# Performance work log

Hardware: AMD Instinct MI355X
Metric: run time of the kernel (lower is better)

The kernel has to match this reference:

```python
import jax, jax.numpy as jnp
import numpy as np

EMB = 256
HEADS = 2
IMG = 224
P1, P2 = 16, 8
LN_EPS = 1e-5


def _layer_norm(t, g, b):
    m = jnp.mean(t, axis=-1, keepdims=True)
    v = jnp.mean((t - m) ** 2, axis=-1, keepdims=True)
    return (t - m) * jax.lax.rsqrt(v + LN_EPS) * g + b


def _patch_embed(x, W, b, cls_tok, p):
    B, C, H, Wd = x.shape
    h, w = H // p, Wd // p
    # b c (h p1)(w p2) -> b (h w) (p1 p2 c)
    t = x.reshape(B, C, h, p, w, p).transpose(0, 2, 4, 3, 5, 1).reshape(B, h * w, p * p * C)
    t = t @ W + b
    cls = jnp.broadcast_to(cls_tok, (B, 1, cls_tok.shape[-1]))
    return jnp.concatenate([cls, t], axis=1)


def setup_inputs() -> dict:
    key = jax.random.key(0)
    ks = jax.random.split(key, 16)
    s = 0.02
    d = {
        "x": jax.random.normal(ks[0], (128, 3, IMG, IMG), dtype=jnp.float32),
        "W1": jax.random.normal(ks[1], (P1 * P1 * 3, EMB), dtype=jnp.float32) * s,
        "b1": jnp.zeros((EMB,), jnp.float32),
        "cls1": jax.random.normal(ks[2], (1, 1, EMB), dtype=jnp.float32),
        "W2": jax.random.normal(ks[3], (P2 * P2 * 3, EMB), dtype=jnp.float32) * s,
        "b2": jnp.zeros((EMB,), jnp.float32),
        "cls2": jax.random.normal(ks[4], (1, 1, EMB), dtype=jnp.float32),
        "ln1_g": jnp.ones((EMB,), jnp.float32),
        "ln1_b": jnp.zeros((EMB,), jnp.float32),
        "Wq": jax.random.normal(ks[5], (EMB, EMB), dtype=jnp.float32) * s,
        "bq": jnp.zeros((EMB,), jnp.float32),
        "Wk": jax.random.normal(ks[6], (EMB, EMB), dtype=jnp.float32) * s,
        "bk": jnp.zeros((EMB,), jnp.float32),
        "Wv": jax.random.normal(ks[7], (EMB, EMB), dtype=jnp.float32) * s,
        "bv": jnp.zeros((EMB,), jnp.float32),
        "Wp": jax.random.normal(ks[8], (EMB, EMB), dtype=jnp.float32) * s,
        "bp": jnp.zeros((EMB,), jnp.float32),
        "ln2_g": jnp.ones((EMB,), jnp.float32),
        "ln2_b": jnp.zeros((EMB,), jnp.float32),
        "lnc_g": jnp.ones((EMB,), jnp.float32),
        "lnc_b": jnp.zeros((EMB,), jnp.float32),
        "Wc": jax.random.normal(ks[9], (EMB, 2), dtype=jnp.float32) * s,
        "bc": jnp.zeros((2,), jnp.float32),
    }
    return d


def reference(x, W1, b1, cls1, W2, b2, cls2, ln1_g, ln1_b, Wq, bq, Wk, bk, Wv, bv,
              Wp, bp, ln2_g, ln2_b, lnc_g, lnc_b, Wc, bc):
    B = x.shape[0]
    p1 = _patch_embed(x, W1, b1, cls1, P1)   # [B, 197, 256]
    p2 = _patch_embed(x, W2, b2, cls2, P2)   # [B, 785, 256]
    n = p1.shape[1]
    idx = jnp.linspace(0.0, p2.shape[1] - 1, n).astype(jnp.int32)  # truncation like .long()
    p2r = p2[:, idx, :]
    z = jnp.concatenate([p2r, p1], axis=1)   # [B, 394, 256]
    N = z.shape[1]

    h = _layer_norm(z, ln1_g, ln1_b)
    dh = EMB // HEADS
    q = (h @ Wq + bq).reshape(B, N, HEADS, dh).transpose(0, 2, 1, 3)
    k = (h @ Wk + bk).reshape(B, N, HEADS, dh).transpose(0, 2, 1, 3)
    v = (h @ Wv + bv).reshape(B, N, HEADS, dh).transpose(0, 2, 1, 3)
    attn = jnp.einsum('bhqd,bhkd->bhqk', q, k)
    # NOTE: faithful to source — softmax of UNscaled logits, then divide by sqrt(emb)
    attn = jax.nn.softmax(attn, axis=-1) / (EMB ** 0.5)
    o = jnp.einsum('bhqk,bhkd->bhqd', attn, v).transpose(0, 2, 1, 3).reshape(B, N, EMB)
    o = o @ Wp + bp
    o = _layer_norm(o, ln2_g, ln2_b)
    z = z + o

    pooled = jnp.mean(z, axis=1)
    logits = _layer_norm(pooled, lnc_g, lnc_b) @ Wc + bc
    return jax.nn.log_softmax(logits, axis=1)
```

## Files before the change

### kernel.cpp

```cpp
#include <hip/hip_runtime.h>

typedef short short8 __attribute__((ext_vector_type(8)));
typedef float f32x4 __attribute__((ext_vector_type(4)));
typedef unsigned short us4 __attribute__((ext_vector_type(4)));
typedef unsigned short u16;

#define MFMA(a,b,c) __builtin_amdgcn_mfma_f32_16x16x32_bf16((a),(b),(c),0,0,0)

__device__ __forceinline__ u16 f2b(float f) {
    union { float f; unsigned int i; } v; v.f = f;
    unsigned int x = v.i;
    return (u16)((x + 0x7fffu + ((x >> 16) & 1u)) >> 16);
}

__device__ __forceinline__ unsigned int pk2(float lo, float hi) {
    return (unsigned int)f2b(lo) | ((unsigned int)f2b(hi) << 16);
}

__global__ __launch_bounds__(256) void k_wtrans(const float* __restrict__ W1,
        const float* __restrict__ W2, const float* __restrict__ Wq, const float* __restrict__ Wk,
        const float* __restrict__ Wv, const float* __restrict__ Wp,
        u16* __restrict__ w1t, u16* __restrict__ w2t, u16* __restrict__ wqt,
        u16* __restrict__ wkt, u16* __restrict__ wvt, u16* __restrict__ wpt) {
    int bx = blockIdx.x, n = threadIdx.x;
    if (bx < 768) {
        int k = bx, c = k % 3, t = k / 3, pj = t & 15, pi = t >> 4;
        int kp2 = c*256 + pi*16 + pj;
        w1t[(size_t)(kp2 >> 5)*8192 + n*32 + (kp2 & 31)] = f2b(W1[(size_t)k*256 + n]);
    } else if (bx < 960) {
        int k = bx - 768, c = k % 3, t = k / 3, pj = t & 7, pi = t >> 3;
        int kp2 = c*64 + pi*8 + pj;
        w2t[(size_t)(kp2 >> 5)*8192 + n*32 + (kp2 & 31)] = f2b(W2[(size_t)k*256 + n]);
    } else if (bx < 1216) { int k = bx - 960;  wqt[(size_t)(k>>5)*8192 + n*32 + (k&31)] = f2b(Wq[(size_t)k*256 + n]); }
    else if (bx < 1472)   { int k = bx - 1216; wkt[(size_t)(k>>5)*8192 + n*32 + (k&31)] = f2b(Wk[(size_t)k*256 + n]); }
    else if (bx < 1728)   { int k = bx - 1472; wvt[(size_t)(k>>5)*8192 + n*32 + (k&31)] = f2b(Wv[(size_t)k*256 + n]); }
    else                  { int k = bx - 1728; wpt[(size_t)(k>>5)*8192 + n*32 + (k&31)] = f2b(Wp[(size_t)k*256 + n]); }
}

__global__ __launch_bounds__(256) void k_cls(const float* __restrict__ cls1,
        const float* __restrict__ cls2, const float* __restrict__ g1, const float* __restrict__ be1,
        float* __restrict__ z, u16* __restrict__ h) {
    __shared__ float red[16];
    int b = blockIdx.x, e = threadIdx.x, lane = e & 63, w = e >> 6;
    float v0 = cls2[e], v1 = cls1[e];
    z[((size_t)b*394 + 0)*256 + e]   = v0;
    z[((size_t)b*394 + 197)*256 + e] = v1;
    float s0 = v0, q0 = v0*v0, s1 = v1, q1 = v1*v1;
    #pragma unroll
    for (int m = 1; m < 64; m <<= 1) {
        s0 += __shfl_xor(s0, m); q0 += __shfl_xor(q0, m);
        s1 += __shfl_xor(s1, m); q1 += __shfl_xor(q1, m);
    }
    if (lane == 0) { red[w] = s0; red[4+w] = q0; red[8+w] = s1; red[12+w] = q1; }
    __syncthreads();
    float S0 = red[0]+red[1]+red[2]+red[3],   Q0 = red[4]+red[5]+red[6]+red[7];
    float S1 = red[8]+red[9]+red[10]+red[11], Q1 = red[12]+red[13]+red[14]+red[15];
    float m0 = S0*(1.f/256.f), r0 = rsqrtf(Q0*(1.f/256.f) - m0*m0 + 1e-5f);
    float m1 = S1*(1.f/256.f), r1 = rsqrtf(Q1*(1.f/256.f) - m1*m1 + 1e-5f);
    h[((size_t)b*394 + 0)*256 + e]   = f2b((v0-m0)*r0*g1[e] + be1[e]);
    h[((size_t)b*394 + 197)*256 + e] = f2b((v1-m1)*r1*g1[e] + be1[e]);
}

__global__ __launch_bounds__(256) void k_im2col1(const float* __restrict__ x,
        u16* __restrict__ A1) {
    int b = blockIdx.y, g = blockIdx.x, tid = threadIdx.x;
    int p = tid >> 4, pi = tid & 15;
    int j = g*16 + p;
    u16* dst = A1 + ((size_t)b*208 + j)*768;
    if (j < 196) {
        int hi = j / 14, wi = j - hi*14;
        #pragma unroll
        for (int c = 0; c < 3; ++c) {
            const float* src = x + (((size_t)b*3 + c)*224 + hi*16 + pi)*224 + wi*16;
            f32x4 r0 = *(const f32x4*)(src);
            f32x4 r1 = *(const f32x4*)(src + 4);
            f32x4 r2 = *(const f32x4*)(src + 8);
            f32x4 r3 = *(const f32x4*)(src + 12);
            union { u16 u[16]; uint4 q[2]; } t;
            #pragma unroll
            for (int s = 0; s < 4; ++s) {
                t.u[s] = f2b(r0[s]); t.u[4+s] = f2b(r1[s]);
                t.u[8+s] = f2b(r2[s]); t.u[12+s] = f2b(r3[s]);
            }
            *(uint4*)&dst[c*256 + pi*16] = t.q[0];
            *(uint4*)&dst[c*256 + pi*16 + 8] = t.q[1];
        }
    } else {
        uint4 zer = {0,0,0,0};
        #pragma unroll
        for (int c = 0; c < 3; ++c) {
            *(uint4*)&dst[c*256 + pi*16] = zer;
            *(uint4*)&dst[c*256 + pi*16 + 8] = zer;
        }
    }
}

__global__ __launch_bounds__(256) void k_embed1(const u16* __restrict__ A1,
        const u16* __restrict__ w1t, const float* __restrict__ b1,
        const float* __restrict__ g1, const float* __restrict__ be1,
        float* __restrict__ z, u16* __restrict__ h, int nrows) {
    __shared__ __align__(16) u16 Ab[2][64*40];
    __shared__ __align__(16) u16 Bb[2][256*40];
    __shared__ float red[64][8];
    int tid = threadIdx.x;
    int r0 = blockIdx.x * 64;
    int w = tid >> 6, lane = tid & 63, quad = lane >> 4, tf = lane & 15;
    int arow = tid >> 2, aoff = (tid & 3) * 8;
    const u16* ap = A1 + (size_t)(r0 + arow)*768 + aoff;
    uint4 ra  = *(const uint4*)(ap);
    uint4 rb0 = *(const uint4*)&w1t[tid*8];
    uint4 rb1 = *(const uint4*)&w1t[2048 + tid*8];
    uint4 rb2 = *(const uint4*)&w1t[4096 + tid*8];
    uint4 rb3 = *(const uint4*)&w1t[6144 + tid*8];
    f32x4 zero = {0.f,0.f,0.f,0.f};
    f32x4 acc[4][4];
    #pragma unroll
    for (int m = 0; m < 4; ++m)
        #pragma unroll
        for (int nf = 0; nf < 4; ++nf) acc[m][nf] = zero;
    #pragma unroll
    for (int kc = 0; kc < 24; ++kc) {
        int buf = kc & 1;
        *(uint4*)&Ab[buf][arow*40 + aoff] = ra;
        *(uint4*)&Bb[buf][(arow      )*40 + aoff] = rb0;
        *(uint4*)&Bb[buf][(arow +  64)*40 + aoff] = rb1;
        *(uint4*)&Bb[buf][(arow + 128)*40 + aoff] = rb2;
        *(uint4*)&Bb[buf][(arow + 192)*40 + aoff] = rb3;
        int nc = kc < 23 ? kc + 1 : 23;
        ra = *(const uint4*)(ap + nc*32);
        const u16* src = w1t + (size_t)nc*8192;
        rb0 = *(const uint4*)&src[tid*8];
        rb1 = *(const uint4*)&src[2048 + tid*8];
        rb2 = *(const uint4*)&src[4096 + tid*8];
        rb3 = *(const uint4*)&src[6144 + tid*8];
        __syncthreads();
        short8 a0 = *(const short8*)&Ab[buf][(     tf)*40 + quad*8];
        short8 a1 = *(const short8*)&Ab[buf][(16 + tf)*40 + quad*8];
        short8 a2 = *(const short8*)&Ab[buf][(32 + tf)*40 + quad*8];
        short8 a3 = *(const short8*)&Ab[buf][(48 + tf)*40 + quad*8];
        #pragma unroll
        for (int nf = 0; nf < 4; ++nf) {
            short8 bb = *(const short8*)&Bb[buf][(w*64 + nf*16 + tf)*40 + quad*8];
            acc[0][nf] = MFMA(a0, bb, acc[0][nf]);
            acc[1][nf] = MFMA(a1, bb, acc[1][nf]);
            acc[2][nf] = MFMA(a2, bb, acc[2][nf]);
            acc[3][nf] = MFMA(a3, bb, acc[3][nf]);
        }
    }
    float bias[4], gv[4], bev[4];
    #pragma unroll
    for (int nf = 0; nf < 4; ++nf) {
        int n = w*64 + nf*16 + tf;
        bias[nf] = b1[n]; gv[nf] = g1[n]; bev[nf] = be1[n];
    }
    #pragma unroll
    for (int m = 0; m < 4; ++m)
        #pragma unroll
        for (int nf = 0; nf < 4; ++nf)
            #pragma unroll
            for (int i = 0; i < 4; ++i) acc[m][nf][i] += bias[nf];
    #pragma unroll
    for (int m = 0; m < 4; ++m)
        #pragma unroll
        for (int i = 0; i < 4; ++i) {
            float s = acc[m][0][i] + acc[m][1][i] + acc[m][2][i] + acc[m][3][i];
            float qv = acc[m][0][i]*acc[m][0][i] + acc[m][1][i]*acc[m][1][i]
                     + acc[m][2][i]*acc[m][2][i] + acc[m][3][i]*acc[m][3][i];
            #pragma unroll
            for (int d = 1; d < 16; d <<= 1) { s += __shfl_xor(s, d); qv += __shfl_xor(qv, d); }
            if (tf == 0) {
                red[m*16 + quad*4 + i][w] = s;
                red[m*16 + quad*4 + i][4 + w] = qv;
            }
        }
    __syncthreads();
    #pragma unroll
    for (int m = 0; m < 4; ++m)
        #pragma unroll
        for (int i = 0; i < 4; ++i) {
            int rl = m*16 + quad*4 + i;
            float S = red[rl][0]+red[rl][1]+red[rl][2]+red[rl][3];
            float Q = red[rl][4]+red[rl][5]+red[rl][6]+red[rl][7];
            float mean = S*(1.f/256.f);
            float rs = rsqrtf(Q*(1.f/256.f) - mean*mean + 1e-5f);
            int row = r0 + rl;
            if (row < nrows) {
                int img = row / 208;
                int j = row - img*208;
                if (j < 196) {
                    size_t base = ((size_t)img*394 + 198 + j)*256;
                    #pragma unroll
                    for (int nf = 0; nf < 4; ++nf) {
                        int n = w*64 + nf*16 + tf;
                        float v = acc[m][nf][i];
                        z[base + n] = v;
                        h[base + n] = f2b((v - mean)*rs*gv[nf] + bev[nf]);
                    }
                }
            }
        }
}

__global__ __launch_bounds__(256) void k_embed2(const float* __restrict__ x,
        const u16* __restrict__ w2t, const float* __restrict__ b2,
        const float* __restrict__ g1, const float* __restrict__ be1,
        float* __restrict__ z, u16* __restrict__ h) {
    __shared__ __align__(16) u16 A[16*200];
    __shared__ __align__(16) u16 Wst[8192];
    __shared__ __align__(16) float S[16*260];
    int b = blockIdx.y, g = blockIdx.x, tid = threadIdx.x;
    int p = tid >> 4, s16 = tid & 15;
    int pi = s16 >> 1, ph = s16 & 1;
    int it = g*16 + p + 1;
    uint4 wr0 = *(const uint4*)&w2t[tid*8];
    uint4 wr1 = *(const uint4*)&w2t[2048 + tid*8];
    uint4 wr2 = *(const uint4*)&w2t[4096 + tid*8];
    uint4 wr3 = *(const uint4*)&w2t[6144 + tid*8];
    auto stage = [&](const u16* base, int chunk) {
        __syncthreads();
        *(uint4*)&Wst[tid*8] = wr0;
        *(uint4*)&Wst[2048 + tid*8] = wr1;
        *(uint4*)&Wst[4096 + tid*8] = wr2;
        *(uint4*)&Wst[6144 + tid*8] = wr3;
        __syncthreads();
        if (base) {
            const u16* src = base + (size_t)chunk*8192;
            wr0 = *(const uint4*)&src[tid*8];
            wr1 = *(const uint4*)&src[2048 + tid*8];
            wr2 = *(const uint4*)&src[4096 + tid*8];
            wr3 = *(const uint4*)&src[6144 + tid*8];
        }
    };
    if (it <= 196) {
        int patch = 4*it - 1;
        int hi = patch / 28, wi = patch - hi*28;
        #pragma unroll
        for (int c = 0; c < 3; ++c) {
            const float* src = x + (((size_t)b*3 + c)*224 + hi*8 + pi)*224 + wi*8 + ph*4;
            f32x4 r = *(const f32x4*)src;
            us4 o; o[0] = f2b(r[0]); o[1] = f2b(r[1]); o[2] = f2b(r[2]); o[3] = f2b(r[3]);
            *(us4*)&A[p*200 + c*64 + pi*8 + ph*4] = o;
        }
    } else {
        us4 zer = {0,0,0,0};
        #pragma unroll
        for (int c = 0; c < 3; ++c)
            *(us4*)&A[p*200 + c*64 + pi*8 + ph*4] = zer;
    }
    int w = tid >> 6, lane = tid & 63, quad = lane >> 4, tf = lane & 15;
    f32x4 zero = {0.f,0.f,0.f,0.f};
    f32x4 acc[4] = {zero,zero,zero,zero};
    #pragma unroll
    for (int ks = 0; ks < 6; ++ks) {
        stage(ks < 5 ? w2t : nullptr, ks + 1);
        short8 a = *(const short8*)&A[tf*200 + ks*32 + quad*8];
        #pragma unroll
        for (int nf = 0; nf < 4; ++nf) {
            short8 bb = *(const short8*)&Wst[(w*64 + nf*16 + tf)*32 + quad*8];
            acc[nf] = MFMA(a, bb, acc[nf]);
        }
    }
    #pragma unroll
    for (int nf = 0; nf < 4; ++nf) {
        int n = w*64 + nf*16 + tf;
        float bias = b2[n];
        #pragma unroll
        for (int i = 0; i < 4; ++i)
            S[(quad*4 + i)*260 + n] = acc[nf][i] + bias;
    }
    __syncthreads();
    #pragma unroll
    for (int rr = 0; rr < 4; ++rr) {
        int row = w*4 + rr;
        int it2 = g*16 + row + 1;
        f32x4 v = *(const f32x4*)&S[row*260 + lane*4];
        float s = v[0]+v[1]+v[2]+v[3];
        float sq = v[0]*v[0]+v[1]*v[1]+v[2]*v[2]+v[3]*v[3];
        #pragma unroll
        for (int m = 1; m < 64; m <<= 1) { s += __shfl_xor(s, m); sq += __shfl_xor(sq, m); }
        float mean = s*(1.f/256.f);
        float rs = rsqrtf(sq*(1.f/256.f) - mean*mean + 1e-5f);
        if (it2 <= 196) {
            size_t base = ((size_t)b*394 + it2)*256 + lane*4;
            *(f32x4*)&z[base] = v;
            us4 ho;
            #pragma unroll
            for (int c = 0; c < 4; ++c) {
                int e = lane*4 + c;
                ho[c] = f2b((v[c]-mean)*rs*g1[e] + be1[e]);
            }
            *(us4*)&h[base] = ho;
        }
    }
}

__device__ __forceinline__ void store_qk(f32x4 acc[4][4], const float* __restrict__ bs,
        u16* __restrict__ dst, u16* Sst, int b, int mt, int w, int quad, int tf, int tid) {
    #pragma unroll
    for (int m = 0; m < 4; ++m) {
        __syncthreads();
        #pragma unroll
        for (int nf = 0; nf < 4; ++nf) {
            int e = w*64 + nf*16 + tf;
            float bias = bs[e];
            #pragma unroll
            for (int i = 0; i < 4; ++i) {
                int n = mt*64 + m*16 + quad*4 + i;
                Sst[(quad*4 + i)*264 + e] = (n < 394) ? f2b(acc[m][nf][i] + bias) : (u16)0;
            }
        }
        __syncthreads();
        int row = tid >> 4, c16 = tid & 15;
        int n = mt*64 + m*16 + row;
        if (n < 416) {
            int e0 = c16*16, hh = e0 >> 7, d0 = e0 & 127;
            uint4 v0 = *(const uint4*)&Sst[row*264 + e0];
            uint4 v1 = *(const uint4*)&Sst[row*264 + e0 + 8];
            u16* p = dst + ((size_t)(b*2 + hh)*416 + n)*128 + d0;
            *(uint4*)p = v0;
            *(uint4*)(p + 8) = v1;
        }
    }
}

__device__ __forceinline__ void store_v(f32x4 acc[4][4], const float* __restrict__ bs,
        u16* __restrict__ vt, u16* Sst, int b, int mt, int w, int quad, int tf, int tid) {
    #pragma unroll
    for (int nf = 0; nf < 4; ++nf) {
        __syncthreads();
        #pragma unroll
        for (int i = 0; i < 4; ++i) {
            int e = w*64 + nf*16 + quad*4 + i;
            float bias = bs[e];
            #pragma unroll
            for (int m = 0; m < 4; ++m) {
                int n = mt*64 + m*16 + tf;
                Sst[(w*16 + quad*4 + i)*72 + m*16 + tf] = (n < 394) ? f2b(acc[m][nf][i] + bias) : (u16)0;
            }
        }
        __syncthreads();
        #pragma unroll
        for (int k = 0; k < 2; ++k) {
            int ch = tid + k*256;
            int row = ch >> 3, c8 = ch & 7;
            int n0 = mt*64 + c8*8;
            if (n0 < 416) {
                int e = (row >> 4)*64 + nf*16 + (row & 15);
                int d = e & 127, hh = e >> 7;
                uint4 v = *(const uint4*)&Sst[row*72 + c8*8];
                *(uint4*)&vt[((size_t)(b*2 + hh)*128 + d)*416 + n0] = v;
            }
        }
    }
}

__global__ __launch_bounds__(256) void k_qkv(const u16* __restrict__ h,
        const u16* __restrict__ wqt, const u16* __restrict__ wkt, const u16* __restrict__ wvt,
        const float* __restrict__ bq, const float* __restrict__ bk, const float* __restrict__ bv,
        u16* __restrict__ q, u16* __restrict__ kb, u16* __restrict__ vt) {
    __shared__ __align__(16) u16 A[64*264];
    __shared__ __align__(16) u16 Wst[8192];
    __shared__ __align__(16) u16 Sst[4608];
    int mt = blockIdx.x, b = blockIdx.y, tid = threadIdx.x;
    uint4 wr0 = *(const uint4*)&wqt[tid*8];
    uint4 wr1 = *(const uint4*)&wqt[2048 + tid*8];
    uint4 wr2 = *(const uint4*)&wqt[4096 + tid*8];
    uint4 wr3 = *(const uint4*)&wqt[6144 + tid*8];
    auto stage = [&](const u16* base, int chunk) {
        __syncthreads();
        *(uint4*)&Wst[tid*8] = wr0;
        *(uint4*)&Wst[2048 + tid*8] = wr1;
        *(uint4*)&Wst[4096 + tid*8] = wr2;
        *(uint4*)&Wst[6144 + tid*8] = wr3;
        __syncthreads();
        if (base) {
            const u16* src = base + (size_t)chunk*8192;
            wr0 = *(const uint4*)&src[tid*8];
            wr1 = *(const uint4*)&src[2048 + tid*8];
            wr2 = *(const uint4*)&src[4096 + tid*8];
            wr3 = *(const uint4*)&src[6144 + tid*8];
        }
    };
    #pragma unroll
    for (int it = 0; it < 8; ++it) {
        int idx = tid + it*256;
        int row = idx >> 5, seg = idx & 31;
        int n = mt*64 + row;
        uint4 val = {0,0,0,0};
        if (n < 394) val = *(const uint4*)&h[((size_t)b*394 + n)*256 + seg*8];
        *(uint4*)&A[row*264 + seg*8] = val;
    }
    int w = tid >> 6, lane = tid & 63, quad = lane >> 4, tf = lane & 15;
    f32x4 zero = {0.f,0.f,0.f,0.f};

    {
        f32x4 acc[4][4];
        #pragma unroll
        for (int m = 0; m < 4; ++m)
            #pragma unroll
            for (int nf = 0; nf < 4; ++nf) acc[m][nf] = zero;
        #pragma unroll
        for (int ks = 0; ks < 8; ++ks) {
            stage(ks < 7 ? wqt : wkt, (ks + 1) & 7);
            short8 a0 = *(const short8*)&A[tf*264 + ks*32 + quad*8];
            short8 a1 = *(const short8*)&A[(16+tf)*264 + ks*32 + quad*8];
            short8 a2 = *(const short8*)&A[(32+tf)*264 + ks*32 + quad*8];
            short8 a3 = *(const short8*)&A[(48+tf)*264 + ks*32 + quad*8];
            #pragma unroll
            for (int nf = 0; nf < 4; ++nf) {
                short8 bb = *(const short8*)&Wst[(w*64 + nf*16 + tf)*32 + quad*8];
                acc[0][nf] = MFMA(a0, bb, acc[0][nf]);
                acc[1][nf] = MFMA(a1, bb, acc[1][nf]);
                acc[2][nf] = MFMA(a2, bb, acc[2][nf]);
                acc[3][nf] = MFMA(a3, bb, acc[3][nf]);
            }
        }
        store_qk(acc, bq, q, Sst, b, mt, w, quad, tf, tid);
    }
    {
        f32x4 acc[4][4];
        #pragma unroll
        for (int m = 0; m < 4; ++m)
            #pragma unroll
            for (int nf = 0; nf < 4; ++nf) acc[m][nf] = zero;
        #pragma unroll
        for (int ks = 0; ks < 8; ++ks) {
            stage(ks < 7 ? wkt : wvt, (ks + 1) & 7);
            short8 a0 = *(const short8*)&A[tf*264 + ks*32 + quad*8];
            short8 a1 = *(const short8*)&A[(16+tf)*264 + ks*32 + quad*8];
            short8 a2 = *(const short8*)&A[(32+tf)*264 + ks*32 + quad*8];
            short8 a3 = *(const short8*)&A[(48+tf)*264 + ks*32 + quad*8];
            #pragma unroll
            for (int nf = 0; nf < 4; ++nf) {
                short8 bb = *(const short8*)&Wst[(w*64 + nf*16 + tf)*32 + quad*8];
                acc[0][nf] = MFMA(a0, bb, acc[0][nf]);
                acc[1][nf] = MFMA(a1, bb, acc[1][nf]);
                acc[2][nf] = MFMA(a2, bb, acc[2][nf]);
                acc[3][nf] = MFMA(a3, bb, acc[3][nf]);
            }
        }
        store_qk(acc, bk, kb, Sst, b, mt, w, quad, tf, tid);
    }
    {
        f32x4 acc[4][4];
        #pragma unroll
        for (int m = 0; m < 4; ++m)
            #pragma unroll
            for (int nf = 0; nf < 4; ++nf) acc[m][nf] = zero;
        #pragma unroll
        for (int ks = 0; ks < 8; ++ks) {
            stage(ks < 7 ? wvt : nullptr, (ks + 1) & 7);
            short8 a0 = *(const short8*)&A[tf*264 + ks*32 + quad*8];
            short8 a1 = *(const short8*)&A[(16+tf)*264 + ks*32 + quad*8];
            short8 a2 = *(const short8*)&A[(32+tf)*264 + ks*32 + quad*8];
            short8 a3 = *(const short8*)&A[(48+tf)*264 + ks*32 + quad*8];
            #pragma unroll
            for (int nf = 0; nf < 4; ++nf) {
                short8 bb = *(const short8*)&Wst[(w*64 + nf*16 + tf)*32 + quad*8];
                acc[0][nf] = MFMA(bb, a0, acc[0][nf]);
                acc[1][nf] = MFMA(bb, a1, acc[1][nf]);
                acc[2][nf] = MFMA(bb, a2, acc[2][nf]);
                acc[3][nf] = MFMA(bb, a3, acc[3][nf]);
            }
        }
        store_v(acc, bv, vt, Sst, b, mt, w, quad, tf, tid);
    }
}

__global__ __launch_bounds__(256) void k_att(const u16* __restrict__ q,
        const u16* __restrict__ kbuf, const u16* __restrict__ vt, u16* __restrict__ o) {
    __shared__ __align__(16) u16 pool[9472];
    u16* Kst = pool;
    u16* Vst = pool + 4352;
    int nwg = gridDim.x * gridDim.y;
    int orig = blockIdx.y * gridDim.x + blockIdx.x;
    int q8 = nwg >> 3, r8 = nwg & 7;
    int xcd = orig & 7, idx = orig >> 3;
    int nid = (xcd < r8 ? xcd*(q8+1) : r8*(q8+1) + (xcd-r8)*q8) + idx;
    int bx = nid % 7, bh = nid / 7;
    int tid = threadIdx.x;
    int w = tid >> 6, lane = tid & 63, quad = lane >> 4, tf = lane & 15;
    int mt_raw = bx*4 + w;
    int mt = mt_raw < 26 ? mt_raw : 25;
    const u16* qp = q    + (size_t)bh*53248;
    const u16* kp = kbuf + (size_t)bh*53248;
    const u16* vp = vt   + (size_t)bh*53248;
    short8 afr[4];
    #pragma unroll
    for (int ks = 0; ks < 4; ++ks)
        afr[ks] = *(const short8*)&qp[(size_t)(mt*16 + tf)*128 + ks*32 + quad*8];
    f32x4 zero = {0.f,0.f,0.f,0.f};
    f32x4 acc[25];
    #pragma unroll
    for (int nt = 0; nt < 25; ++nt) acc[nt] = zero;
    int sr0 = tid >> 4, sseg = tid & 15;
    uint4 kreg0 = *(const uint4*)&kp[(size_t)sr0*128 + sseg*8];
    uint4 kreg1 = *(const uint4*)&kp[(size_t)(sr0+16)*128 + sseg*8];
    for (int kc = 0; kc < 13; ++kc) {
        __syncthreads();
        *(uint4*)&Kst[sr0*136 + sseg*8] = kreg0;
        *(uint4*)&Kst[(sr0+16)*136 + sseg*8] = kreg1;
        __syncthreads();
        if (kc < 12) {
            kreg0 = *(const uint4*)&kp[(size_t)((kc+1)*32 + sr0)*128 + sseg*8];
            kreg1 = *(const uint4*)&kp[(size_t)((kc+1)*32 + sr0 + 16)*128 + sseg*8];
        }
        #pragma unroll
        for (int ncl = 0; ncl < 2; ++ncl) {
            int nt = kc*2 + ncl;
            if (nt < 25) {
                #pragma unroll
                for (int ks = 0; ks < 4; ++ks) {
                    short8 kk = *(const short8*)&Kst[(ncl*16 + tf)*136 + ks*32 + quad*8];
                    acc[nt] = MFMA(kk, afr[ks], acc[nt]);
                }
            }
        }
    }
    int vd0 = tid >> 2, vseg = tid & 3;
    uint4 vreg0 = *(const uint4*)&vp[(size_t)vd0*416 + vseg*8];
    uint4 vreg1 = *(const uint4*)&vp[(size_t)(vd0+64)*416 + vseg*8];
    float mx = -3e38f;
    #pragma unroll
    for (int nt = 0; nt < 24; ++nt)
        #pragma unroll
        for (int i = 0; i < 4; ++i) mx = fmaxf(mx, acc[nt][i]);
    #pragma unroll
    for (int i = 0; i < 4; ++i)
        if (quad*4 + i < 10) mx = fmaxf(mx, acc[24][i]);
    mx = fmaxf(mx, __shfl_xor(mx, 16));
    mx = fmaxf(mx, __shfl_xor(mx, 32));
    float s = 0.f;
    #pragma unroll
    for (int nt = 0; nt < 24; ++nt)
        #pragma unroll
        for (int i = 0; i < 4; ++i) {
            float e = __expf(acc[nt][i] - mx);
            acc[nt][i] = e; s += e;
        }
    #pragma unroll
    for (int i = 0; i < 4; ++i) {
        if (quad*4 + i < 10) { float e = __expf(acc[24][i] - mx); acc[24][i] = e; s += e; }
        else acc[24][i] = 0.f;
    }
    s += __shfl_xor(s, 16);
    s += __shfl_xor(s, 32);
    float inv = 1.f / (16.f * s);
    #pragma unroll
    for (int nt = 0; nt < 25; ++nt)
        #pragma unroll
        for (int i = 0; i < 4; ++i) acc[nt][i] *= inv;
    f32x4 acc2[8];
    #pragma unroll
    for (int nf = 0; nf < 8; ++nf) acc2[nf] = zero;
    int qb0 = quad & 1;
    int g = (qb0 << 1) | (quad >> 1);
    for (int kc = 0; kc < 13; ++kc) {
        __syncthreads();
        *(uint4*)&Vst[vd0*40 + vseg*8] = vreg0;
        *(uint4*)&Vst[(vd0+64)*40 + vseg*8] = vreg1;
        __syncthreads();
        if (kc < 12) {
            vreg0 = *(const uint4*)&vp[(size_t)vd0*416 + (kc+1)*32 + vseg*8];
            vreg1 = *(const uint4*)&vp[(size_t)(vd0+64)*416 + (kc+1)*32 + vseg*8];
        }
        f32x4 v0 = acc[2*kc];
        f32x4 v1 = (kc < 12) ? acc[2*kc + 1] : zero;
        unsigned int r0 = pk2(v0[0], v0[1]);
        unsigned int r1 = pk2(v0[2], v0[3]);
        unsigned int r2 = pk2(v1[0], v1[1]);
        unsigned int r3 = pk2(v1[2], v1[3]);
        unsigned int sa = qb0 ? r0 : r2, sb = qb0 ? r1 : r3;
        unsigned int ra = (unsigned int)__shfl_xor((int)sa, 16);
        unsigned int rb = (unsigned int)__shfl_xor((int)sb, 16);
        unsigned int ka = qb0 ? r2 : r0, kb2 = qb0 ? r3 : r1;
        union { unsigned int u[4]; short8 s8; } au;
        au.u[0] = qb0 ? ra : ka;
        au.u[1] = qb0 ? rb : kb2;
        au.u[2] = qb0 ? ka : ra;
        au.u[3] = qb0 ? kb2 : rb;
        short8 a = au.s8;
        #pragma unroll
        for (int nf = 0; nf < 8; ++nf) {
            short8 bb = *(const short8*)&Vst[(nf*16 + tf)*40 + g*8];
            acc2[nf] = MFMA(a, bb, acc2[nf]);
        }
    }
    int b = bh >> 1, hh = bh & 1;
    __syncthreads();
    #pragma unroll
    for (int nf = 0; nf < 8; ++nf)
        #pragma unroll
        for (int i = 0; i < 4; ++i)
            pool[w*2176 + (quad*4 + i)*136 + nf*16 + tf] = f2b(acc2[nf][i]);
    __syncthreads();
    if (mt_raw < 26) {
        #pragma unroll
        for (int r4 = 0; r4 < 4; ++r4) {
            int rr = r4*4 + (lane >> 4);
            int n = mt_raw*16 + rr;
            if (n < 394) {
                int c16 = lane & 15;
                uint4 v = *(const uint4*)&pool[w*2176 + rr*136 + c16*8];
                *(uint4*)&o[((size_t)b*394 + n)*256 + hh*128 + c16*8] = v;
            }
        }
    }
}

__global__ __launch_bounds__(256) void k_proj(const u16* __restrict__ o,
        const u16* __restrict__ wpt, const float* __restrict__ bp,
        const float* __restrict__ g2, const float* __restrict__ bb2,
        float* __restrict__ z) {
    __shared__ __align__(16) u16 A[32*264];
    __shared__ __align__(16) u16 Wst[8192];
    __shared__ __align__(16) float S[32*260];
    int mt = blockIdx.x, b = blockIdx.y, tid = threadIdx.x;
    int w = tid >> 6, lane = tid & 63, quad = lane >> 4, tf = lane & 15;
    uint4 wr0 = *(const uint4*)&wpt[tid*8];
    uint4 wr1 = *(const uint4*)&wpt[2048 + tid*8];
    uint4 wr2 = *(const uint4*)&wpt[4096 + tid*8];
    uint4 wr3 = *(const uint4*)&wpt[6144 + tid*8];
    auto stage = [&](const u16* base, int chunk) {
        __syncthreads();
        *(uint4*)&Wst[tid*8] = wr0;
        *(uint4*)&Wst[2048 + tid*8] = wr1;
        *(uint4*)&Wst[4096 + tid*8] = wr2;
        *(uint4*)&Wst[6144 + tid*8] = wr3;
        __syncthreads();
        if (base) {
            const u16* src = base + (size_t)chunk*8192;
            wr0 = *(const uint4*)&src[tid*8];
            wr1 = *(const uint4*)&src[2048 + tid*8];
            wr2 = *(const uint4*)&src[4096 + tid*8];
            wr3 = *(const uint4*)&src[6144 + tid*8];
        }
    };
    for (int idx = tid; idx < 2048; idx += 256) {
        int row = idx >> 6, col4 = (idx & 63) * 4;
        int n = mt*32 + row;
        us4 val = {0,0,0,0};
        if (n < 394) val = *(const us4*)&o[((size_t)b*394 + n)*256 + col4];
        *(us4*)&A[row*264 + col4] = val;
    }
    f32x4 zero = {0.f,0.f,0.f,0.f};
    f32x4 acc[2][4];
    #pragma unroll
    for (int m = 0; m < 2; ++m)
        #pragma unroll
        for (int nf = 0; nf < 4; ++nf) acc[m][nf] = zero;
    #pragma unroll
    for (int ks = 0; ks < 8; ++ks) {
        stage(ks < 7 ? wpt : nullptr, ks + 1);
        short8 a0 = *(const short8*)&A[tf*264 + ks*32 + quad*8];
        short8 a1 = *(const short8*)&A[(16+tf)*264 + ks*32 + quad*8];
        #pragma unroll
        for (int nf = 0; nf < 4; ++nf) {
            short8 bb = *(const short8*)&Wst[(w*64 + nf*16 + tf)*32 + quad*8];
            acc[0][nf] = MFMA(a0, bb, acc[0][nf]);
            acc[1][nf] = MFMA(a1, bb, acc[1][nf]);
        }
    }
    #pragma unroll
    for (int nf = 0; nf < 4; ++nf) {
        int e = w*64 + nf*16 + tf;
        float bsv = bp[e];
        #pragma unroll
        for (int m = 0; m < 2; ++m)
            #pragma unroll
            for (int i = 0; i < 4; ++i)
                S[(m*16 + quad*4 + i)*260 + e] = acc[m][nf][i] + bsv;
    }
    __syncthreads();
    #pragma unroll
    for (int rr = 0; rr < 8; ++rr) {
        int row = w*8 + rr;
        f32x4 v = *(const f32x4*)&S[row*260 + lane*4];
        float s = v[0]+v[1]+v[2]+v[3];
        float sq = v[0]*v[0]+v[1]*v[1]+v[2]*v[2]+v[3]*v[3];
        #pragma unroll
        for (int m = 1; m < 64; m <<= 1) { s += __shfl_xor(s, m); sq += __shfl_xor(sq, m); }
        float mean = s*(1.f/256.f);
        float rs = rsqrtf(sq*(1.f/256.f) - mean*mean + 1e-5f);
        int n = mt*32 + row;
        if (n < 394) {
            float* zr = z + ((size_t)b*394 + n)*256 + lane*4;
            f32x4 zv = *(f32x4*)zr;
            #pragma unroll
            for (int c = 0; c < 4; ++c) {
                int e = lane*4 + c;
                zv[c] += (v[c]-mean)*rs*g2[e] + bb2[e];
            }
            *(f32x4*)zr = zv;
        }
    }
}

__global__ __launch_bounds__(256) void k_pool(const float* __restrict__ z,
        const float* __restrict__ lg, const float* __restrict__ lb,
        const float* __restrict__ wc, const float* __restrict__ bc,
        float* __restrict__ out) {
    __shared__ float red[8];
    int b = blockIdx.x, e = threadIdx.x;
    int wave = e >> 6, lane = e & 63;
    const float* zp = z + (size_t)b*394*256 + e;
    float p0 = 0.f, p1 = 0.f, p2 = 0.f, p3 = 0.f;
    int n = 0;
    for (; n + 3 < 394; n += 4) {
        p0 += zp[(size_t)n*256];       p1 += zp[(size_t)(n+1)*256];
        p2 += zp[(size_t)(n+2)*256];   p3 += zp[(size_t)(n+3)*256];
    }
    for (; n < 394; ++n) p0 += zp[(size_t)n*256];
    float pooled = (p0+p1+p2+p3) * (1.f/394.f);
    float a = pooled, sq = pooled*pooled;
    #pragma unroll
    for (int m = 1; m < 64; m <<= 1) { a += __shfl_xor(a, m); sq += __shfl_xor(sq, m); }
    if (lane == 0) { red[wave] = a; red[4+wave] = sq; }
    __syncthreads();
    float tot = red[0]+red[1]+red[2]+red[3];
    float totq = red[4]+red[5]+red[6]+red[7];
    float mean = tot*(1.f/256.f);
    float rs = rsqrtf(totq*(1.f/256.f) - mean*mean + 1e-5f);
    float ln = (pooled-mean)*rs*lg[e] + lb[e];
    float t0 = ln * wc[e*2], t1 = ln * wc[e*2+1];
    #pragma unroll
    for (int m = 1; m < 64; m <<= 1) { t0 += __shfl_xor(t0, m); t1 += __shfl_xor(t1, m); }
    __syncthreads();
    if (lane == 0) { red[wave] = t0; red[4+wave] = t1; }
    __syncthreads();
    if (e < 2) {
        float l0 = red[0]+red[1]+red[2]+red[3] + bc[0];
        float l1 = red[4]+red[5]+red[6]+red[7] + bc[1];
        float mx = fmaxf(l0, l1);
        float lse = mx + logf(__expf(l0-mx) + __expf(l1-mx));
        out[b*2 + e] = (e == 0 ? l0 : l1) - lse;
    }
}

extern "C" void kernel_launch(void* const* d_in, const int* in_sizes, int n_in,
                              void* d_out, int out_size, void* d_ws, size_t ws_size,
                              hipStream_t stream) {
    const float* x    = (const float*)d_in[0];
    const float* W1   = (const float*)d_in[1];
    const float* b1   = (const float*)d_in[2];
    const float* cls1 = (const float*)d_in[3];
    const float* W2   = (const float*)d_in[4];
    const float* b2   = (const float*)d_in[5];
    const float* cls2 = (const float*)d_in[6];
    const float* ln1g = (const float*)d_in[7];
    const float* ln1b = (const float*)d_in[8];
    const float* Wq   = (const float*)d_in[9];
    const float* bq   = (const float*)d_in[10];
    const float* Wk   = (const float*)d_in[11];
    const float* bk   = (const float*)d_in[12];
    const float* Wv   = (const float*)d_in[13];
    const float* bv   = (const float*)d_in[14];
    const float* Wp   = (const float*)d_in[15];
    const float* bp   = (const float*)d_in[16];
    const float* ln2g = (const float*)d_in[17];
    const float* ln2b = (const float*)d_in[18];
    const float* lncg = (const float*)d_in[19];
    const float* lncb = (const float*)d_in[20];
    const float* Wc   = (const float*)d_in[21];
    const float* bcp  = (const float*)d_in[22];

    int Bn = in_sizes[0] / (3*224*224);

    const size_t WBYTES = 1015808;
    const size_t PER_IMG = 403456 + 201728 + 212992*3;
    size_t avail = (ws_size > WBYTES) ? ws_size - WBYTES : 0;
    int Bc = (int)(avail / PER_IMG);
    if (Bc < 1) Bc = 1;
    if (Bc > Bn) Bc = Bn;

    u16* w1t = (u16*)d_ws;
    u16* w2t = w1t + 196608;
    u16* wqt = w2t + 49152;
    u16* wkt = wqt + 65536;
    u16* wvt = wkt + 65536;
    u16* wpt = wvt + 65536;
    float* z = (float*)(wpt + 65536);
    u16* h   = (u16*)(z + (size_t)Bc*100864);
    u16* o   = h;
    u16* q   = h + (size_t)Bc*100864;
    u16* kb  = q + (size_t)Bc*106496;
    u16* vt  = kb + (size_t)Bc*106496;

    k_wtrans<<<1984, 256, 0, stream>>>(W1, W2, Wq, Wk, Wv, Wp, w1t, w2t, wqt, wkt, wvt, wpt);

    for (int b0 = 0; b0 < Bn; b0 += Bc) {
        int bc = (Bn - b0 < Bc) ? (Bn - b0) : Bc;
        const float* xb = x + (size_t)b0 * 3*224*224;
        float* outb = (float*)d_out + (size_t)b0 * 2;
        int nrows = bc * 208;
        int gm = (nrows + 63) / 64;

        k_cls<<<bc, 256, 0, stream>>>(cls1, cls2, ln1g, ln1b, z, h);
        k_im2col1<<<dim3(13, bc), 256, 0, stream>>>(xb, q );
        k_embed1<<<gm, 256, 0, stream>>>(q , w1t, b1, ln1g, ln1b, z, h, nrows);
        k_embed2<<<dim3(13, bc), 256, 0, stream>>>(xb, w2t, b2, ln1g, ln1b, z, h);
        k_qkv<<<dim3(7, bc), 256, 0, stream>>>(h, wqt, wkt, wvt, bq, bk, bv, q, kb, vt);
        k_att<<<dim3(7, bc*2), 256, 0, stream>>>(q, kb, vt, o);
        k_proj<<<dim3(13, bc), 256, 0, stream>>>(o, wpt, bp, ln2g, ln2b, z);
        k_pool<<<bc, 256, 0, stream>>>(z, lncg, lncb, Wc, bcp, outb);
    }
}
```

Baseline: 391.2 us.

## Double-buffer LDS staging in qkv/attention and split pooling reduction across blocks

In k_qkv and k_att, weight, K and V tiles are now staged into two alternating LDS buffers. This removes one of the two barriers per iteration and lets the next global prefetch run before the barrier. The pooling kernel is split into a partial-sum kernel over four row groups per image plus a finalize kernel, which adds parallelism to the pooling read of z. In exchange, LDS usage per block doubles in attention, and there is an extra kernel launch plus a small workspace buffer for the partial sums.

Measured after the change: 379.9 us. 2.9% less time.

```diff
diff --git a/kernel.cpp b/kernel.cpp
--- a/kernel.cpp
+++ b/kernel.cpp
@@ -359,27 +359,24 @@
         const float* __restrict__ bq, const float* __restrict__ bk, const float* __restrict__ bv,
         u16* __restrict__ q, u16* __restrict__ kb, u16* __restrict__ vt) {
     __shared__ __align__(16) u16 A[64*264];
-    __shared__ __align__(16) u16 Wst[8192];
+    __shared__ __align__(16) u16 Wst[2][8192];
     __shared__ __align__(16) u16 Sst[4608];
     int mt = blockIdx.x, b = blockIdx.y, tid = threadIdx.x;
     uint4 wr0 = *(const uint4*)&wqt[tid*8];
     uint4 wr1 = *(const uint4*)&wqt[2048 + tid*8];
     uint4 wr2 = *(const uint4*)&wqt[4096 + tid*8];
     uint4 wr3 = *(const uint4*)&wqt[6144 + tid*8];
-    auto stage = [&](const u16* base, int chunk) {
-        __syncthreads();
-        *(uint4*)&Wst[tid*8] = wr0;
-        *(uint4*)&Wst[2048 + tid*8] = wr1;
-        *(uint4*)&Wst[4096 + tid*8] = wr2;
-        *(uint4*)&Wst[6144 + tid*8] = wr3;
-        __syncthreads();
-        if (base) {
-            const u16* src = base + (size_t)chunk*8192;
-            wr0 = *(const uint4*)&src[tid*8];
-            wr1 = *(const uint4*)&src[2048 + tid*8];
-            wr2 = *(const uint4*)&src[4096 + tid*8];
-            wr3 = *(const uint4*)&src[6144 + tid*8];
-        }
+    auto wwrite = [&](int buf) {
+        *(uint4*)&Wst[buf][tid*8] = wr0;
+        *(uint4*)&Wst[buf][2048 + tid*8] = wr1;
+        *(uint4*)&Wst[buf][4096 + tid*8] = wr2;
+        *(uint4*)&Wst[buf][6144 + tid*8] = wr3;
+    };
+    auto wload = [&](const u16* src) {
+        wr0 = *(const uint4*)&src[tid*8];
+        wr1 = *(const uint4*)&src[2048 + tid*8];
+        wr2 = *(const uint4*)&src[4096 + tid*8];
+        wr3 = *(const uint4*)&src[6144 + tid*8];
     };
     #pragma unroll
     for (int it = 0; it < 8; ++it) {
@@ -401,14 +398,17 @@
             for (int nf = 0; nf < 4; ++nf) acc[m][nf] = zero;
         #pragma unroll
         for (int ks = 0; ks < 8; ++ks) {
-            stage(ks < 7 ? wqt : wkt, (ks + 1) & 7);
+            int buf = ks & 1;
+            wwrite(buf);
+            wload(ks < 7 ? wqt + (size_t)(ks+1)*8192 : wkt);
+            __syncthreads();
             short8 a0 = *(const short8*)&A[tf*264 + ks*32 + quad*8];
             short8 a1 = *(const short8*)&A[(16+tf)*264 + ks*32 + quad*8];
             short8 a2 = *(const short8*)&A[(32+tf)*264 + ks*32 + quad*8];
             short8 a3 = *(const short8*)&A[(48+tf)*264 + ks*32 + quad*8];
             #pragma unroll
             for (int nf = 0; nf < 4; ++nf) {
-                short8 bb = *(const short8*)&Wst[(w*64 + nf*16 + tf)*32 + quad*8];
+                short8 bb = *(const short8*)&Wst[buf][(w*64 + nf*16 + tf)*32 + quad*8];
                 acc[0][nf] = MFMA(a0, bb, acc[0][nf]);
                 acc[1][nf] = MFMA(a1, bb, acc[1][nf]);
                 acc[2][nf] = MFMA(a2, bb, acc[2][nf]);
@@ -425,14 +425,17 @@
             for (int nf = 0; nf < 4; ++nf) acc[m][nf] = zero;
         #pragma unroll
         for (int ks = 0; ks < 8; ++ks) {
-            stage(ks < 7 ? wkt : wvt, (ks + 1) & 7);
+            int buf = ks & 1;
+            wwrite(buf);
+            wload(ks < 7 ? wkt + (size_t)(ks+1)*8192 : wvt);
+            __syncthreads();
             short8 a0 = *(const short8*)&A[tf*264 + ks*32 + quad*8];
             short8 a1 = *(const short8*)&A[(16+tf)*264 + ks*32 + quad*8];
             short8 a2 = *(const short8*)&A[(32+tf)*264 + ks*32 + quad*8];
             short8 a3 = *(const short8*)&A[(48+tf)*264 + ks*32 + quad*8];
             #pragma unroll
             for (int nf = 0; nf < 4; ++nf) {
-                short8 bb = *(const short8*)&Wst[(w*64 + nf*16 + tf)*32 + quad*8];
+                short8 bb = *(const short8*)&Wst[buf][(w*64 + nf*16 + tf)*32 + quad*8];
                 acc[0][nf] = MFMA(a0, bb, acc[0][nf]);
                 acc[1][nf] = MFMA(a1, bb, acc[1][nf]);
                 acc[2][nf] = MFMA(a2, bb, acc[2][nf]);
@@ -449,14 +452,17 @@
             for (int nf = 0; nf < 4; ++nf) acc[m][nf] = zero;
         #pragma unroll
         for (int ks = 0; ks < 8; ++ks) {
-            stage(ks < 7 ? wvt : nullptr, (ks + 1) & 7);
+            int buf = ks & 1;
+            wwrite(buf);
+            if (ks < 7) wload(wvt + (size_t)(ks+1)*8192);
+            __syncthreads();
             short8 a0 = *(const short8*)&A[tf*264 + ks*32 + quad*8];
             short8 a1 = *(const short8*)&A[(16+tf)*264 + ks*32 + quad*8];
             short8 a2 = *(const short8*)&A[(32+tf)*264 + ks*32 + quad*8];
             short8 a3 = *(const short8*)&A[(48+tf)*264 + ks*32 + quad*8];
             #pragma unroll
             for (int nf = 0; nf < 4; ++nf) {
-                short8 bb = *(const short8*)&Wst[(w*64 + nf*16 + tf)*32 + quad*8];
+                short8 bb = *(const short8*)&Wst[buf][(w*64 + nf*16 + tf)*32 + quad*8];
                 acc[0][nf] = MFMA(bb, a0, acc[0][nf]);
                 acc[1][nf] = MFMA(bb, a1, acc[1][nf]);
                 acc[2][nf] = MFMA(bb, a2, acc[2][nf]);
@@ -469,9 +475,7 @@
 
 __global__ __launch_bounds__(256) void k_att(const u16* __restrict__ q,
         const u16* __restrict__ kbuf, const u16* __restrict__ vt, u16* __restrict__ o) {
-    __shared__ __align__(16) u16 pool[9472];
-    u16* Kst = pool;
-    u16* Vst = pool + 4352;
+    __shared__ __align__(16) u16 pool[18944];
     int nwg = gridDim.x * gridDim.y;
     int orig = blockIdx.y * gridDim.x + blockIdx.x;
     int q8 = nwg >> 3, r8 = nwg & 7;
@@ -497,21 +501,21 @@
     uint4 kreg0 = *(const uint4*)&kp[(size_t)sr0*128 + sseg*8];
     uint4 kreg1 = *(const uint4*)&kp[(size_t)(sr0+16)*128 + sseg*8];
     for (int kc = 0; kc < 13; ++kc) {
-        __syncthreads();
-        *(uint4*)&Kst[sr0*136 + sseg*8] = kreg0;
-        *(uint4*)&Kst[(sr0+16)*136 + sseg*8] = kreg1;
-        __syncthreads();
+        u16* K = pool + (kc & 1)*4352;
+        *(uint4*)&K[sr0*136 + sseg*8] = kreg0;
+        *(uint4*)&K[(sr0+16)*136 + sseg*8] = kreg1;
         if (kc < 12) {
             kreg0 = *(const uint4*)&kp[(size_t)((kc+1)*32 + sr0)*128 + sseg*8];
             kreg1 = *(const uint4*)&kp[(size_t)((kc+1)*32 + sr0 + 16)*128 + sseg*8];
         }
+        __syncthreads();
         #pragma unroll
         for (int ncl = 0; ncl < 2; ++ncl) {
             int nt = kc*2 + ncl;
             if (nt < 25) {
                 #pragma unroll
                 for (int ks = 0; ks < 4; ++ks) {
-                    short8 kk = *(const short8*)&Kst[(ncl*16 + tf)*136 + ks*32 + quad*8];
+                    short8 kk = *(const short8*)&K[(ncl*16 + tf)*136 + ks*32 + quad*8];
                     acc[nt] = MFMA(kk, afr[ks], acc[nt]);
                 }
             }
@@ -556,14 +560,14 @@
     int qb0 = quad & 1;
     int g = (qb0 << 1) | (quad >> 1);
     for (int kc = 0; kc < 13; ++kc) {
-        __syncthreads();
-        *(uint4*)&Vst[vd0*40 + vseg*8] = vreg0;
-        *(uint4*)&Vst[(vd0+64)*40 + vseg*8] = vreg1;
-        __syncthreads();
+        u16* V = pool + 8704 + (kc & 1)*5120;
+        *(uint4*)&V[vd0*40 + vseg*8] = vreg0;
+        *(uint4*)&V[(vd0+64)*40 + vseg*8] = vreg1;
         if (kc < 12) {
             vreg0 = *(const uint4*)&vp[(size_t)vd0*416 + (kc+1)*32 + vseg*8];
             vreg1 = *(const uint4*)&vp[(size_t)(vd0+64)*416 + (kc+1)*32 + vseg*8];
         }
+        __syncthreads();
         f32x4 v0 = acc[2*kc];
         f32x4 v1 = (kc < 12) ? acc[2*kc + 1] : zero;
         unsigned int r0 = pk2(v0[0], v0[1]);
@@ -582,7 +586,7 @@
         short8 a = au.s8;
         #pragma unroll
         for (int nf = 0; nf < 8; ++nf) {
-            short8 bb = *(const short8*)&Vst[(nf*16 + tf)*40 + g*8];
+            short8 bb = *(const short8*)&V[(nf*16 + tf)*40 + g*8];
             acc2[nf] = MFMA(a, bb, acc2[nf]);
         }
     }
@@ -696,22 +700,32 @@
     }
 }
 
-__global__ __launch_bounds__(256) void k_pool(const float* __restrict__ z,
+__global__ __launch_bounds__(256) void k_poolsum(const float* __restrict__ z,
+        float* __restrict__ partial) {
+    int g = blockIdx.x, b = blockIdx.y, e = threadIdx.x;
+    int nb = gridDim.y;
+    int n0 = g*99, n1 = 394 < n0+99 ? 394 : n0+99;
+    const float* zp = z + (size_t)b*394*256 + e;
+    float p0 = 0.f, p1 = 0.f, p2 = 0.f, p3 = 0.f;
+    int n = n0;
+    for (; n + 3 < n1; n += 4) {
+        p0 += zp[(size_t)n*256];       p1 += zp[(size_t)(n+1)*256];
+        p2 += zp[(size_t)(n+2)*256];   p3 += zp[(size_t)(n+3)*256];
+    }
+    for (; n < n1; ++n) p0 += zp[(size_t)n*256];
+    partial[((size_t)g*nb + b)*256 + e] = (p0+p1)+(p2+p3);
+}
+
+__global__ __launch_bounds__(256) void k_pool2(const float* __restrict__ partial,
         const float* __restrict__ lg, const float* __restrict__ lb,
         const float* __restrict__ wc, const float* __restrict__ bc,
-        float* __restrict__ out) {
+        float* __restrict__ out, int nb) {
     __shared__ float red[8];
     int b = blockIdx.x, e = threadIdx.x;
     int wave = e >> 6, lane = e & 63;
-    const float* zp = z + (size_t)b*394*256 + e;
-    float p0 = 0.f, p1 = 0.f, p2 = 0.f, p3 = 0.f;
-    int n = 0;
-    for (; n + 3 < 394; n += 4) {
-        p0 += zp[(size_t)n*256];       p1 += zp[(size_t)(n+1)*256];
-        p2 += zp[(size_t)(n+2)*256];   p3 += zp[(size_t)(n+3)*256];
-    }
-    for (; n < 394; ++n) p0 += zp[(size_t)n*256];
-    float pooled = (p0+p1+p2+p3) * (1.f/394.f);
+    float pooled = (partial[((size_t)0*nb + b)*256 + e] + partial[((size_t)1*nb + b)*256 + e]
+                  + partial[((size_t)2*nb + b)*256 + e] + partial[((size_t)3*nb + b)*256 + e])
+                 * (1.f/394.f);
     float a = pooled, sq = pooled*pooled;
     #pragma unroll
     for (int m = 1; m < 64; m <<= 1) { a += __shfl_xor(a, m); sq += __shfl_xor(sq, m); }
@@ -767,7 +781,7 @@
     int Bn = in_sizes[0] / (3*224*224);
 
     const size_t WBYTES = 1015808;
-    const size_t PER_IMG = 403456 + 201728 + 212992*3;
+    const size_t PER_IMG = 403456 + 201728 + 212992*3 + 4096;
     size_t avail = (ws_size > WBYTES) ? ws_size - WBYTES : 0;
     int Bc = (int)(avail / PER_IMG);
     if (Bc < 1) Bc = 1;
@@ -785,6 +799,7 @@
     u16* q   = h + (size_t)Bc*100864;
     u16* kb  = q + (size_t)Bc*106496;
     u16* vt  = kb + (size_t)Bc*106496;
+    float* partial = (float*)(vt + (size_t)Bc*106496);
 
     k_wtrans<<<1984, 256, 0, stream>>>(W1, W2, Wq, Wk, Wv, Wp, w1t, w2t, wqt, wkt, wvt, wpt);
 
@@ -802,6 +817,7 @@
         k_qkv<<<dim3(7, bc), 256, 0, stream>>>(h, wqt, wkt, wvt, bq, bk, bv, q, kb, vt);
         k_att<<<dim3(7, bc*2), 256, 0, stream>>>(q, kb, vt, o);
         k_proj<<<dim3(13, bc), 256, 0, stream>>>(o, wpt, bp, ln2g, ln2b, z);
-        k_pool<<<bc, 256, 0, stream>>>(z, lncg, lncb, Wc, bcp, outb);
-    }
-}
+        k_poolsum<<<dim3(4, bc), 256, 0, stream>>>(z, partial);
+        k_pool2<<<bc, 256, 0, stream>>>(partial, lncg, lncb, Wc, bcp, outb, bc);
+    }
+}
```
